# Optimization experiments

Measured on AMD Instinct MI355X. Metric: run time of the kernel, lower is better.

Reference implementation:

```python
import jax, jax.numpy as jnp
import numpy as np

EPS = 1e-6
LN_EPS = 1e-5


def setup_inputs() -> dict:
    key = jax.random.key(0)
    k1, k2, k3 = jax.random.split(key, 3)
    N, L, H, D = 4, 16384, 8, 16
    return {
        "queries": jax.random.normal(k1, (N, L, H, D), dtype=jnp.float32),
        "keys": jax.random.normal(k2, (N, L, H, D), dtype=jnp.float32),
        "values": jax.random.normal(k3, (N, L, H, D), dtype=jnp.float32),
        "ln_gamma": jnp.ones((D,), dtype=jnp.float32),
        "ln_beta": jnp.zeros((D,), dtype=jnp.float32),
    }


def reference(queries, keys, values, ln_gamma, ln_beta):
    initial = values  # [N, L, H, D]
    # to [N, H, L, D] and apply sigmoid feature map
    q = jax.nn.sigmoid(jnp.transpose(queries, (0, 2, 1, 3)))
    k = jax.nn.sigmoid(jnp.transpose(keys, (0, 2, 1, 3)))
    v = jnp.transpose(values, (0, 2, 1, 3))
    L = q.shape[2]
    S = k.shape[2]
    # competition/allocation normalizers (flow attention)
    normalizer_row = 1.0 / jnp.einsum('nhld,nhd->nhl', q + EPS, k.sum(axis=2) + EPS)
    normalizer_col = 1.0 / jnp.einsum('nhsd,nhd->nhs', k + EPS, q.sum(axis=2) + EPS)
    normalizer_row_refine = jnp.einsum(
        'nhld,nhd->nhl', q + EPS, (k * normalizer_col[..., None]).sum(axis=2) + EPS)
    normalizer_col_refine = jnp.einsum(
        'nhsd,nhd->nhs', k + EPS, (q * normalizer_row[..., None]).sum(axis=2) + EPS)
    normalizer_row_refine = jax.nn.sigmoid(normalizer_row_refine * (float(L) / float(S)))
    normalizer_col_refine = jax.nn.softmax(normalizer_col_refine, axis=-1) * S
    # linear attention: K^T @ (V * col_refine), then Q @ kv
    kv = jnp.einsum('nhsd,nhse->nhde', k, v * normalizer_col_refine[..., None])  # [N,H,D,D]
    x = jnp.einsum('nhld,nhde->nhle', q, kv)
    x = x * normalizer_row[..., None] * normalizer_row_refine[..., None]
    x = jnp.transpose(x, (0, 2, 1, 3))  # [N, L, H, D]
    x = initial + x
    # LayerNorm over last dim (D=16), biased variance as in torch
    mean = jnp.mean(x, axis=-1, keepdims=True)
    var = jnp.mean(jnp.square(x - mean), axis=-1, keepdims=True)
    x = (x - mean) / jnp.sqrt(var + LN_EPS) * ln_gamma + ln_beta
    return x
```

## Files before the change

kernel.cpp:

```cpp
#include <hip/hip_runtime.h>
#include <math.h>
#include <stdint.h>

constexpr int LL = 16384;
constexpr int NROW = 65536;
constexpr int NPAIR = NROW * 8;
constexpr int PAIRS_PER_N = NPAIR / 4;
constexpr float EPS = 1e-6f;
constexpr float LN_EPS = 1e-5f;

constexpr int F_KSUM = 0;
constexpr int F_KN   = 512;
constexpr int F_SS   = 1024;
constexpr int F_QSUM = 1056;
constexpr int F_QN   = 1568;
constexpr int F_KV   = 2080;
constexpr int P_A1 = 10272;
constexpr int P_A2 = P_A1 + 2048 * 256;
constexpr int P_KN = P_A2 + 2048 * 128;
constexpr int P_SS = P_KN + 2048 * 128;
constexpr int P_KV = P_SS + 2048 * 8;
constexpr int FLOAT_END = P_KV + 2048 * 2048;
constexpr size_t MIR_Q_BYTE = (size_t)FLOAT_END * 4;
constexpr size_t MIR_ELEMS  = (size_t)NPAIR * 16;
constexpr size_t MIR_K_BYTE = MIR_Q_BYTE + MIR_ELEMS * 2;
constexpr size_t WS_FULL    = MIR_K_BYTE + MIR_ELEMS * 2;

__device__ __forceinline__ float sigm(float x) { return __fdividef(1.f, 1.f + __expf(-x)); }
__device__ __forceinline__ unsigned short f2bf(float f) {
  uint32_t x = __float_as_uint(f);
  return (unsigned short)((x + 0x7FFFu + ((x >> 16) & 1u)) >> 16);
}
__device__ __forceinline__ float bf2f(unsigned short u) {
  return __uint_as_float(((uint32_t)u) << 16);
}

template <bool MIR>
__device__ __forceinline__ void load_sig(const unsigned short* mir, const float* fp, int p, float* r) {
  if (MIR) {
    const uint4* p4 = reinterpret_cast<const uint4*>(mir + (size_t)p * 16);
    uint4 a = p4[0], b = p4[1];
    uint32_t w[8] = {a.x, a.y, a.z, a.w, b.x, b.y, b.z, b.w};
#pragma unroll
    for (int j = 0; j < 8; ++j) {
      r[2 * j]     = bf2f((unsigned short)(w[j] & 0xFFFFu));
      r[2 * j + 1] = bf2f((unsigned short)(w[j] >> 16));
    }
  } else {
    const float4* p4 = reinterpret_cast<const float4*>(fp + (size_t)p * 16);
#pragma unroll
    for (int j = 0; j < 4; ++j) {
      float4 a = p4[j];
      r[4 * j] = sigm(a.x); r[4 * j + 1] = sigm(a.y);
      r[4 * j + 2] = sigm(a.z); r[4 * j + 3] = sigm(a.w);
    }
  }
}
__device__ __forceinline__ void load_raw16(const float* fp, int p, float* r) {
  const float4* p4 = reinterpret_cast<const float4*>(fp + (size_t)p * 16);
#pragma unroll
  for (int j = 0; j < 4; ++j) {
    float4 a = p4[j];
    r[4 * j] = a.x; r[4 * j + 1] = a.y; r[4 * j + 2] = a.z; r[4 * j + 3] = a.w;
  }
}

__device__ __forceinline__ float hred(float v) {
  v += __shfl_xor(v, 8, 64);
  v += __shfl_xor(v, 16, 64);
  v += __shfl_xor(v, 32, 64);
  return v;
}

__device__ __forceinline__ void stat_partial2(float* a, float* b, float* w4 ,
                                              float* dst, int tid) {
  const int wave = tid >> 6, lane = tid & 63;
#pragma unroll
  for (int d = 0; d < 16; ++d) { a[d] = hred(a[d]); b[d] = hred(b[d]); }
  if (lane < 8) {
#pragma unroll
    for (int d = 0; d < 16; ++d) {
      w4[wave * 256 + lane * 16 + d] = a[d];
      w4[wave * 256 + 128 + lane * 16 + d] = b[d];
    }
  }
  __syncthreads();
  dst[tid] = w4[tid] + w4[256 + tid] + w4[512 + tid] + w4[768 + tid];
}

__device__ __forceinline__ void stat_partial1(float* a, float* w1 ,
                                              float* dst, int tid) {
  const int wave = tid >> 6, lane = tid & 63;
#pragma unroll
  for (int d = 0; d < 16; ++d) a[d] = hred(a[d]);
  if (lane < 8) {
#pragma unroll
    for (int d = 0; d < 16; ++d) w1[wave * 128 + lane * 16 + d] = a[d];
  }
  __syncthreads();
  if (tid < 128) dst[tid] = w1[tid] + w1[128 + tid] + w1[256 + tid] + w1[384 + tid];
}

template <bool MIR>
__global__ __launch_bounds__(256) void k_prep(const float* __restrict__ Q, const float* __restrict__ K,
                                              float* __restrict__ ws,
                                              unsigned short* __restrict__ sQ, unsigned short* __restrict__ sK) {
  const int tid = threadIdx.x;
  const int p = blockIdx.x * 256 + tid;
  __shared__ float w4[1024];
  float q[16], k[16];
  load_sig<false>(nullptr, Q, p, q);
  load_sig<false>(nullptr, K, p, k);
  if (MIR) {
    union U { unsigned short u[8]; uint4 v; };
    U a, bb;
#pragma unroll
    for (int j = 0; j < 8; ++j) { a.u[j] = f2bf(q[j]); bb.u[j] = f2bf(q[8 + j]); }
    uint4* dq = reinterpret_cast<uint4*>(sQ + (size_t)p * 16);
    dq[0] = a.v; dq[1] = bb.v;
#pragma unroll
    for (int j = 0; j < 8; ++j) { a.u[j] = f2bf(k[j]); bb.u[j] = f2bf(k[8 + j]); }
    uint4* dk = reinterpret_cast<uint4*>(sK + (size_t)p * 16);
    dk[0] = a.v; dk[1] = bb.v;
  }
  stat_partial2(q, k, w4, ws + P_A1 + (size_t)blockIdx.x * 256, tid);
}

__global__ __launch_bounds__(256) void k_redA(float* __restrict__ ws) {
  const int tid = threadIdx.x;
  const int n = blockIdx.x >> 3, seg = blockIdx.x & 7;
  const int el = tid & 31, sub = tid >> 5;
  __shared__ float w[256];
  const float* src = ws + P_A1 + ((size_t)(n * 512 + sub * 64)) * 256 + seg * 32 + el;
  float a = 0.f;
#pragma unroll
  for (int i = 0; i < 64; ++i) a += src[(size_t)i * 256];
  w[tid] = a;
  __syncthreads();
  if (tid < 128) w[tid] += w[tid + 128];
  __syncthreads();
  if (tid < 64) w[tid] += w[tid + 64];
  __syncthreads();
  if (tid < 32) {
    const float v = w[tid] + w[tid + 32];
    const int elem = seg * 32 + tid;
    if (elem < 128) ws[F_QSUM + n * 128 + elem] = v;
    else ws[F_KSUM + n * 128 + (elem - 128)] = v;
  }
}

template <bool MIR>
__global__ __launch_bounds__(256) void k_refq(const float* __restrict__ Q,
                                              const unsigned short* __restrict__ sQ,
                                              float* __restrict__ ws) {
  const int tid = threadIdx.x;
  const int p = blockIdx.x * 256 + tid;
  const int n = blockIdx.x >> 9;
  __shared__ float ksE[128];
  __shared__ float w1[512];
  if (tid < 128) ksE[tid] = ws[F_KSUM + n * 128 + tid] + EPS;
  __syncthreads();
  const int h = tid & 7;
  float q[16];
  load_sig<MIR>(sQ, Q, p, q);
  float dr = 0.f;
#pragma unroll
  for (int d = 0; d < 16; ++d) dr += (q[d] + EPS) * ksE[h * 16 + d];
  const float nr = __fdividef(1.f, dr);
#pragma unroll
  for (int d = 0; d < 16; ++d) q[d] *= nr;
  stat_partial1(q, w1, ws + P_A2 + (size_t)blockIdx.x * 128, tid);
}

__global__ __launch_bounds__(256) void k_redB(float* __restrict__ ws) {
  const int tid = threadIdx.x;
  const int n = blockIdx.x >> 2, seg = blockIdx.x & 3;
  const int el = tid & 31, sub = tid >> 5;
  __shared__ float w[256];
  const float* src = ws + P_A2 + ((size_t)(n * 512 + sub * 64)) * 128 + seg * 32 + el;
  float a = 0.f;
#pragma unroll
  for (int i = 0; i < 64; ++i) a += src[(size_t)i * 128];
  w[tid] = a;
  __syncthreads();
  if (tid < 128) w[tid] += w[tid + 128];
  __syncthreads();
  if (tid < 64) w[tid] += w[tid + 64];
  __syncthreads();
  if (tid < 32) ws[F_QN + n * 128 + seg * 32 + tid] = w[tid] + w[tid + 32];
}

template <bool MIR>
__global__ __launch_bounds__(256) void k_kv(const float* __restrict__ K, const float* __restrict__ V,
                                            const unsigned short* __restrict__ sK,
                                            float* __restrict__ ws) {
  const int tid = threadIdx.x;
  const int blk = blockIdx.x;
  const int n = blk >> 9;
  constexpr int RS = 132;
  __shared__ float qnE[128], qsE[128];
  __shared__ float ssb[8];
  __shared__ float w1[512];
  __shared__ __align__(16) float kwL[32 * RS];
  __shared__ __align__(16) float vL[32 * RS];
  if (tid < 128) {
    qnE[tid] = ws[F_QN + n * 128 + tid] + EPS;
    qsE[tid] = ws[F_QSUM + n * 128 + tid] + EPS;
  }
  if (tid < 8) ssb[tid] = 0.f;
  __syncthreads();
  const int h = tid & 7, ri = tid >> 3, lane = tid & 63;
  const int h2 = tid >> 5;
  const int d0 = ((tid >> 2) & 7) * 2;
  const int e0 = (tid & 3) * 4;
  const int p = blk * 256 + tid;
  float k[16], v[16];
  load_sig<MIR>(sK, K, p, k);
  load_raw16(V, p, v);
  float dc = 0.f, ncr = 0.f;
#pragma unroll
  for (int d = 0; d < 16; ++d) {
    const float ke = k[d] + EPS;
    dc += ke * qsE[h * 16 + d];
    ncr += ke * qnE[h * 16 + d];
  }
  const float nc = __fdividef(1.f, dc);
  float kn[16];
#pragma unroll
  for (int d = 0; d < 16; ++d) kn[d] = k[d] * nc;
  const float w = __expf(ncr);
  float sw = hred(w);
  if (lane < 8) atomicAdd(&ssb[lane], sw);
  const int wb = ri * RS + h * 16;
#pragma unroll
  for (int d = 0; d < 16; ++d) { kwL[wb + d] = k[d] * w; vL[wb + d] = v[d]; }
  __syncthreads();
  float acc[2][4] = {{0.f, 0.f, 0.f, 0.f}, {0.f, 0.f, 0.f, 0.f}};
  const int rb0 = h2 * 16;
#pragma unroll 4
  for (int r = 0; r < 32; ++r) {
    const int rb = r * RS + rb0;
    const float2 kk = *reinterpret_cast<const float2*>(&kwL[rb + d0]);
    const float4 vv = *reinterpret_cast<const float4*>(&vL[rb + e0]);
    acc[0][0] += kk.x * vv.x; acc[0][1] += kk.x * vv.y;
    acc[0][2] += kk.x * vv.z; acc[0][3] += kk.x * vv.w;
    acc[1][0] += kk.y * vv.x; acc[1][1] += kk.y * vv.y;
    acc[1][2] += kk.y * vv.z; acc[1][3] += kk.y * vv.w;
  }
  __syncthreads();
  stat_partial1(kn, w1, ws + P_KN + (size_t)blk * 128, tid);
  if (tid < 8) ws[P_SS + (size_t)blk * 8 + tid] = ssb[tid];
  float* pk = ws + P_KV + (size_t)blk * 2048;
  *reinterpret_cast<float4*>(pk + h2 * 256 + d0 * 16 + e0) =
      make_float4(acc[0][0], acc[0][1], acc[0][2], acc[0][3]);
  *reinterpret_cast<float4*>(pk + h2 * 256 + (d0 + 1) * 16 + e0) =
      make_float4(acc[1][0], acc[1][1], acc[1][2], acc[1][3]);
}

__global__ __launch_bounds__(256) void k_redC(float* __restrict__ ws) {
  const int tid = threadIdx.x;
  const int blk = blockIdx.x;
  __shared__ float w[256];
  if (blk < 256) {
    const int n = blk >> 6, seg = blk & 63;
    const int el = tid & 31, sub = tid >> 5;
    const float* src = ws + P_KV + ((size_t)(n * 512 + sub * 64)) * 2048 + seg * 32 + el;
    float a = 0.f;
#pragma unroll
    for (int i = 0; i < 64; ++i) a += src[(size_t)i * 2048];
    w[tid] = a;
    __syncthreads();
    if (tid < 128) w[tid] += w[tid + 128];
    __syncthreads();
    if (tid < 64) w[tid] += w[tid + 64];
    __syncthreads();
    if (tid < 32) ws[F_KV + n * 2048 + seg * 32 + tid] = w[tid] + w[tid + 32];
  } else if (blk < 272) {
    const int b2 = blk - 256;
    const int n = b2 >> 2, seg = b2 & 3;
    const int el = tid & 31, sub = tid >> 5;
    const float* src = ws + P_KN + ((size_t)(n * 512 + sub * 64)) * 128 + seg * 32 + el;
    float a = 0.f;
#pragma unroll
    for (int i = 0; i < 64; ++i) a += src[(size_t)i * 128];
    w[tid] = a;
    __syncthreads();
    if (tid < 128) w[tid] += w[tid + 128];
    __syncthreads();
    if (tid < 64) w[tid] += w[tid + 64];
    __syncthreads();
    if (tid < 32) ws[F_KN + n * 128 + seg * 32 + tid] = w[tid] + w[tid + 32];
  } else {
    const int n = blk - 272;
    const int h = tid & 7, sub = tid >> 3;
    const float* src = ws + P_SS + ((size_t)(n * 512 + sub * 16)) * 8 + h;
    float a = 0.f;
#pragma unroll
    for (int i = 0; i < 16; ++i) a += src[(size_t)i * 8];
    w[tid] = a;
    __syncthreads();
    if (tid < 128) w[tid] += w[tid + 128];
    __syncthreads();
    if (tid < 64) w[tid] += w[tid + 64];
    __syncthreads();
    if (tid < 32) w[tid] += w[tid + 32];
    __syncthreads();
    if (tid < 16) w[tid] += w[tid + 16];
    __syncthreads();
    if (tid < 8) ws[F_SS + n * 8 + tid] = w[tid] + w[tid + 8];
  }
}

template <bool MIR>
__global__ __launch_bounds__(256) void k_out(const float* __restrict__ Q, const float* __restrict__ V,
                                             const unsigned short* __restrict__ sQ,
                                             const float* __restrict__ gamma, const float* __restrict__ beta,
                                             const float* __restrict__ ws, float* __restrict__ out) {
  const int tid = threadIdx.x;
  const int p = blockIdx.x * 256 + tid;
  const int n = blockIdx.x >> 9;
  __shared__ __align__(16) float kvs[8 * 260];
  __shared__ float ksE[128], knE[128], gm[16], bt[16], ssE[8];
  if (tid < 8) ssE[tid] = __fdividef((float)LL, ws[F_SS + n * 8 + tid]);
  if (tid >= 8 && tid < 136) {
    const int i = tid - 8;
    ksE[i] = ws[F_KSUM + n * 128 + i] + EPS;
    knE[i] = ws[F_KN + n * 128 + i] + EPS;
  }
  if (tid >= 136 && tid < 152) gm[tid - 136] = gamma[tid - 136];
  else if (tid >= 152 && tid < 168) bt[tid - 152] = beta[tid - 152];
  __syncthreads();
  for (int i = tid; i < 2048; i += 256) {
    const int hh = i >> 8, de = i & 255;
    kvs[hh * 260 + de] = ws[F_KV + n * 2048 + i] * ssE[hh];
  }
  __syncthreads();
  const int h = tid & 7;
  float q[16], v[16];
  load_sig<MIR>(sQ, Q, p, q);
  load_raw16(V, p, v);
  float dr = 0.f, drr = 0.f;
#pragma unroll
  for (int d = 0; d < 16; ++d) {
    const float qe = q[d] + EPS;
    dr += qe * ksE[h * 16 + d];
    drr += qe * knE[h * 16 + d];
  }
  const float sc = __fdividef(1.f, dr) * sigm(drr);
  float x[16];
#pragma unroll
  for (int e = 0; e < 16; ++e) x[e] = 0.f;
#pragma unroll
  for (int d = 0; d < 16; ++d) {
    const float qd = q[d];
    const float4* kr = reinterpret_cast<const float4*>(&kvs[h * 260 + d * 16]);
#pragma unroll
    for (int j = 0; j < 4; ++j) {
      float4 a = kr[j];
      x[4 * j] += qd * a.x; x[4 * j + 1] += qd * a.y;
      x[4 * j + 2] += qd * a.z; x[4 * j + 3] += qd * a.w;
    }
  }
#pragma unroll
  for (int e = 0; e < 16; ++e) x[e] = x[e] * sc + v[e];
  float mean = 0.f;
#pragma unroll
  for (int e = 0; e < 16; ++e) mean += x[e];
  mean *= (1.f / 16.f);
  float var = 0.f;
#pragma unroll
  for (int e = 0; e < 16; ++e) { const float t = x[e] - mean; var += t * t; }
  var *= (1.f / 16.f);
  const float inv = rsqrtf(var + LN_EPS);
#pragma unroll
  for (int e = 0; e < 16; ++e) x[e] = (x[e] - mean) * inv * gm[e] + bt[e];
  float4* op = reinterpret_cast<float4*>(out + (size_t)p * 16);
  op[0] = make_float4(x[0], x[1], x[2], x[3]);
  op[1] = make_float4(x[4], x[5], x[6], x[7]);
  op[2] = make_float4(x[8], x[9], x[10], x[11]);
  op[3] = make_float4(x[12], x[13], x[14], x[15]);
}

extern "C" void kernel_launch(void* const* d_in, const int* in_sizes, int n_in,
                              void* d_out, int out_size, void* d_ws, size_t ws_size,
                              hipStream_t stream) {
  const float* Q = (const float*)d_in[0];
  const float* K = (const float*)d_in[1];
  const float* V = (const float*)d_in[2];
  const float* gamma = (const float*)d_in[3];
  const float* beta = (const float*)d_in[4];
  float* ws = (float*)d_ws;
  float* out = (float*)d_out;
  unsigned short* sQ = (unsigned short*)((char*)d_ws + MIR_Q_BYTE);
  unsigned short* sK = (unsigned short*)((char*)d_ws + MIR_K_BYTE);

  const dim3 blk(256);
  const int gBig = NPAIR / 256;

  if (ws_size >= WS_FULL) {
    k_prep<true><<<gBig, blk, 0, stream>>>(Q, K, ws, sQ, sK);
    k_redA<<<32, blk, 0, stream>>>(ws);
    k_refq<true><<<gBig, blk, 0, stream>>>(Q, sQ, ws);
    k_redB<<<16, blk, 0, stream>>>(ws);
    k_kv<true><<<gBig, blk, 0, stream>>>(K, V, sK, ws);
    k_redC<<<276, blk, 0, stream>>>(ws);
    k_out<true><<<gBig, blk, 0, stream>>>(Q, V, sQ, gamma, beta, ws, out);
  } else {
    k_prep<false><<<gBig, blk, 0, stream>>>(Q, K, ws, nullptr, nullptr);
    k_redA<<<32, blk, 0, stream>>>(ws);
    k_refq<false><<<gBig, blk, 0, stream>>>(Q, nullptr, ws);
    k_redB<<<16, blk, 0, stream>>>(ws);
    k_kv<false><<<gBig, blk, 0, stream>>>(K, V, nullptr, ws);
    k_redC<<<276, blk, 0, stream>>>(ws);
    k_out<false><<<gBig, blk, 0, stream>>>(Q, V, nullptr, gamma, beta, ws, out);
  }
}
```

Measured before the change: 200.6 us.

## Stage per-row global loads and stores through padded LDS for coalescing

Every kernel (prep, refq, kv, out) now loads its 256-row tile of Q/K/V with consecutive threads reading consecutive float4/uint2 chunks into a padded LDS buffer, then each thread reads its own 16-element row from LDS. The bf16 mirror writes and the final output stores take the same route in reverse. Before, each thread read and wrote a 64-byte row stride. The aim is fully coalesced global access, paid for with extra LDS traffic, more __syncthreads, and larger shared-memory use that may lower occupancy.

After: 206.7 us. 1.03x slower.

```diff
diff --git a/kernel.cpp b/kernel.cpp
--- a/kernel.cpp
+++ b/kernel.cpp
@@ -5,9 +5,9 @@
 constexpr int LL = 16384;
 constexpr int NROW = 65536;
 constexpr int NPAIR = NROW * 8;
-constexpr int PAIRS_PER_N = NPAIR / 4;
 constexpr float EPS = 1e-6f;
 constexpr float LN_EPS = 1e-5f;
+constexpr size_t MIR_ELEMS = (size_t)NPAIR * 16;
 
 constexpr int F_KSUM = 0;
 constexpr int F_KN   = 512;
@@ -22,9 +22,9 @@
 constexpr int P_KV = P_SS + 2048 * 8;
 constexpr int FLOAT_END = P_KV + 2048 * 2048;
 constexpr size_t MIR_Q_BYTE = (size_t)FLOAT_END * 4;
-constexpr size_t MIR_ELEMS  = (size_t)NPAIR * 16;
 constexpr size_t MIR_K_BYTE = MIR_Q_BYTE + MIR_ELEMS * 2;
 constexpr size_t WS_FULL    = MIR_K_BYTE + MIR_ELEMS * 2;
+
 
 __device__ __forceinline__ float sigm(float x) { return __fdividef(1.f, 1.f + __expf(-x)); }
 __device__ __forceinline__ unsigned short f2bf(float f) {
@@ -35,33 +35,42 @@
   return __uint_as_float(((uint32_t)u) << 16);
 }
 
-template <bool MIR>
-__device__ __forceinline__ void load_sig(const unsigned short* mir, const float* fp, int p, float* r) {
-  if (MIR) {
-    const uint4* p4 = reinterpret_cast<const uint4*>(mir + (size_t)p * 16);
-    uint4 a = p4[0], b = p4[1];
-    uint32_t w[8] = {a.x, a.y, a.z, a.w, b.x, b.y, b.z, b.w};
-#pragma unroll
-    for (int j = 0; j < 8; ++j) {
-      r[2 * j]     = bf2f((unsigned short)(w[j] & 0xFFFFu));
-      r[2 * j + 1] = bf2f((unsigned short)(w[j] >> 16));
-    }
-  } else {
-    const float4* p4 = reinterpret_cast<const float4*>(fp + (size_t)p * 16);
-#pragma unroll
-    for (int j = 0; j < 4; ++j) {
-      float4 a = p4[j];
-      r[4 * j] = sigm(a.x); r[4 * j + 1] = sigm(a.y);
-      r[4 * j + 2] = sigm(a.z); r[4 * j + 3] = sigm(a.w);
-    }
-  }
-}
-__device__ __forceinline__ void load_raw16(const float* fp, int p, float* r) {
-  const float4* p4 = reinterpret_cast<const float4*>(fp + (size_t)p * 16);
-#pragma unroll
-  for (int j = 0; j < 4; ++j) {
-    float4 a = p4[j];
-    r[4 * j] = a.x; r[4 * j + 1] = a.y; r[4 * j + 2] = a.z; r[4 * j + 3] = a.w;
+
+__device__ __forceinline__ void stage_f32(const float* src, int pairBase, float* lds, int tid) {
+  const float4* s4 = reinterpret_cast<const float4*>(src) + (size_t)pairBase * 4;
+#pragma unroll
+  for (int i = 0; i < 4; ++i) {
+    const int G = i * 256 + tid;
+    const float4 v = s4[G];
+    float* r = lds + (G >> 2) * 17 + (G & 3) * 4;
+    r[0] = v.x; r[1] = v.y; r[2] = v.z; r[3] = v.w;
+  }
+}
+
+__device__ __forceinline__ void stage_bf16(const unsigned short* mir, int pairBase, float* lds, int tid) {
+  const uint2* s2 = reinterpret_cast<const uint2*>(mir) + (size_t)pairBase * 4;
+#pragma unroll
+  for (int i = 0; i < 4; ++i) {
+    const int G = i * 256 + tid;
+    const uint2 u = s2[G];
+    float* r = lds + (G >> 2) * 17 + (G & 3) * 4;
+    r[0] = bf2f((unsigned short)(u.x & 0xFFFFu)); r[1] = bf2f((unsigned short)(u.x >> 16));
+    r[2] = bf2f((unsigned short)(u.y & 0xFFFFu)); r[3] = bf2f((unsigned short)(u.y >> 16));
+  }
+}
+
+__device__ __forceinline__ void mirror_store(unsigned short* mir, int pairBase, uint32_t* ldsu,
+                                             const float* q, int tid) {
+#pragma unroll
+  for (int j = 0; j < 8; ++j)
+    ldsu[tid * 9 + j] = (uint32_t)f2bf(q[2 * j]) | ((uint32_t)f2bf(q[2 * j + 1]) << 16);
+  __syncthreads();
+  uint2* d2 = reinterpret_cast<uint2*>(mir) + (size_t)pairBase * 4;
+#pragma unroll
+  for (int i = 0; i < 4; ++i) {
+    const int G = i * 256 + tid;
+    const int pl = G >> 2, qd = G & 3;
+    d2[G] = make_uint2(ldsu[pl * 9 + qd * 2], ldsu[pl * 9 + qd * 2 + 1]);
   }
 }
 
@@ -106,24 +115,29 @@
                                               float* __restrict__ ws,
                                               unsigned short* __restrict__ sQ, unsigned short* __restrict__ sK) {
   const int tid = threadIdx.x;
-  const int p = blockIdx.x * 256 + tid;
-  __shared__ float w4[1024];
+  const int pairBase = blockIdx.x * 256;
+  __shared__ __align__(16) float A[4352];
+  uint32_t* Au = reinterpret_cast<uint32_t*>(A);
   float q[16], k[16];
-  load_sig<false>(nullptr, Q, p, q);
-  load_sig<false>(nullptr, K, p, k);
+  stage_f32(Q, pairBase, A, tid);
+  __syncthreads();
+#pragma unroll
+  for (int d = 0; d < 16; ++d) q[d] = sigm(A[tid * 17 + d]);
+  __syncthreads();
   if (MIR) {
-    union U { unsigned short u[8]; uint4 v; };
-    U a, bb;
-#pragma unroll
-    for (int j = 0; j < 8; ++j) { a.u[j] = f2bf(q[j]); bb.u[j] = f2bf(q[8 + j]); }
-    uint4* dq = reinterpret_cast<uint4*>(sQ + (size_t)p * 16);
-    dq[0] = a.v; dq[1] = bb.v;
-#pragma unroll
-    for (int j = 0; j < 8; ++j) { a.u[j] = f2bf(k[j]); bb.u[j] = f2bf(k[8 + j]); }
-    uint4* dk = reinterpret_cast<uint4*>(sK + (size_t)p * 16);
-    dk[0] = a.v; dk[1] = bb.v;
-  }
-  stat_partial2(q, k, w4, ws + P_A1 + (size_t)blockIdx.x * 256, tid);
+    mirror_store(sQ, pairBase, Au, q, tid);
+    __syncthreads();
+  }
+  stage_f32(K, pairBase, A, tid);
+  __syncthreads();
+#pragma unroll
+  for (int d = 0; d < 16; ++d) k[d] = sigm(A[tid * 17 + d]);
+  __syncthreads();
+  if (MIR) {
+    mirror_store(sK, pairBase, Au, k, tid);
+    __syncthreads();
+  }
+  stat_partial2(q, k, A, ws + P_A1 + (size_t)blockIdx.x * 256, tid);
 }
 
 __global__ __launch_bounds__(256) void k_redA(float* __restrict__ ws) {
@@ -154,22 +168,29 @@
                                               const unsigned short* __restrict__ sQ,
                                               float* __restrict__ ws) {
   const int tid = threadIdx.x;
-  const int p = blockIdx.x * 256 + tid;
+  const int pairBase = blockIdx.x * 256;
   const int n = blockIdx.x >> 9;
+  __shared__ __align__(16) float A[4352];
   __shared__ float ksE[128];
   __shared__ float w1[512];
+  if (MIR) stage_bf16(sQ, pairBase, A, tid);
+  else     stage_f32(Q, pairBase, A, tid);
   if (tid < 128) ksE[tid] = ws[F_KSUM + n * 128 + tid] + EPS;
   __syncthreads();
   const int h = tid & 7;
-  float q[16];
-  load_sig<MIR>(sQ, Q, p, q);
+  float qv[16];
+#pragma unroll
+  for (int d = 0; d < 16; ++d) {
+    const float t = A[tid * 17 + d];
+    qv[d] = MIR ? t : sigm(t);
+  }
   float dr = 0.f;
 #pragma unroll
-  for (int d = 0; d < 16; ++d) dr += (q[d] + EPS) * ksE[h * 16 + d];
+  for (int d = 0; d < 16; ++d) dr += (qv[d] + EPS) * ksE[h * 16 + d];
   const float nr = __fdividef(1.f, dr);
 #pragma unroll
-  for (int d = 0; d < 16; ++d) q[d] *= nr;
-  stat_partial1(q, w1, ws + P_A2 + (size_t)blockIdx.x * 128, tid);
+  for (int d = 0; d < 16; ++d) qv[d] *= nr;
+  stat_partial1(qv, w1, ws + P_A2 + (size_t)blockIdx.x * 128, tid);
 }
 
 __global__ __launch_bounds__(256) void k_redB(float* __restrict__ ws) {
@@ -200,23 +221,59 @@
   constexpr int RS = 132;
   __shared__ float qnE[128], qsE[128];
   __shared__ float ssb[8];
-  __shared__ float w1[512];
   __shared__ __align__(16) float kwL[32 * RS];
   __shared__ __align__(16) float vL[32 * RS];
+  const int pairBase = blk * 256;
+  if (MIR) {
+    const uint2* s2 = reinterpret_cast<const uint2*>(sK) + (size_t)pairBase * 4;
+#pragma unroll
+    for (int i = 0; i < 4; ++i) {
+      const int G = i * 256 + tid;
+      const uint2 u = s2[G];
+      const int p = G >> 2;
+      float* r = &kwL[(p >> 3) * RS + (p & 7) * 16 + (G & 3) * 4];
+      r[0] = bf2f((unsigned short)(u.x & 0xFFFFu)); r[1] = bf2f((unsigned short)(u.x >> 16));
+      r[2] = bf2f((unsigned short)(u.y & 0xFFFFu)); r[3] = bf2f((unsigned short)(u.y >> 16));
+    }
+  } else {
+    const float4* s4 = reinterpret_cast<const float4*>(K) + (size_t)pairBase * 4;
+#pragma unroll
+    for (int i = 0; i < 4; ++i) {
+      const int G = i * 256 + tid;
+      const float4 v4 = s4[G];
+      const int p = G >> 2;
+      float* r = &kwL[(p >> 3) * RS + (p & 7) * 16 + (G & 3) * 4];
+      r[0] = v4.x; r[1] = v4.y; r[2] = v4.z; r[3] = v4.w;
+    }
+  }
+  {
+    const float4* s4 = reinterpret_cast<const float4*>(V) + (size_t)pairBase * 4;
+#pragma unroll
+    for (int i = 0; i < 4; ++i) {
+      const int G = i * 256 + tid;
+      const float4 v4 = s4[G];
+      const int p = G >> 2;
+      float* r = &vL[(p >> 3) * RS + (p & 7) * 16 + (G & 3) * 4];
+      r[0] = v4.x; r[1] = v4.y; r[2] = v4.z; r[3] = v4.w;
+    }
+  }
   if (tid < 128) {
     qnE[tid] = ws[F_QN + n * 128 + tid] + EPS;
     qsE[tid] = ws[F_QSUM + n * 128 + tid] + EPS;
   }
   if (tid < 8) ssb[tid] = 0.f;
   __syncthreads();
-  const int h = tid & 7, ri = tid >> 3, lane = tid & 63;
+  const int h = tid & 7, lane = tid & 63;
   const int h2 = tid >> 5;
   const int d0 = ((tid >> 2) & 7) * 2;
   const int e0 = (tid & 3) * 4;
-  const int p = blk * 256 + tid;
-  float k[16], v[16];
-  load_sig<MIR>(sK, K, p, k);
-  load_raw16(V, p, v);
+  const int myrow = (tid >> 3) * RS + h * 16;
+  float k[16];
+#pragma unroll
+  for (int d = 0; d < 16; ++d) {
+    const float t = kwL[myrow + d];
+    k[d] = MIR ? t : sigm(t);
+  }
   float dc = 0.f, ncr = 0.f;
 #pragma unroll
   for (int d = 0; d < 16; ++d) {
@@ -231,9 +288,8 @@
   const float w = __expf(ncr);
   float sw = hred(w);
   if (lane < 8) atomicAdd(&ssb[lane], sw);
-  const int wb = ri * RS + h * 16;
-#pragma unroll
-  for (int d = 0; d < 16; ++d) { kwL[wb + d] = k[d] * w; vL[wb + d] = v[d]; }
+#pragma unroll
+  for (int d = 0; d < 16; ++d) kwL[myrow + d] = k[d] * w;
   __syncthreads();
   float acc[2][4] = {{0.f, 0.f, 0.f, 0.f}, {0.f, 0.f, 0.f, 0.f}};
   const int rb0 = h2 * 16;
@@ -248,7 +304,7 @@
     acc[1][2] += kk.y * vv.z; acc[1][3] += kk.y * vv.w;
   }
   __syncthreads();
-  stat_partial1(kn, w1, ws + P_KN + (size_t)blk * 128, tid);
+  stat_partial1(kn, kwL, ws + P_KN + (size_t)blk * 128, tid);
   if (tid < 8) ws[P_SS + (size_t)blk * 8 + tid] = ssb[tid];
   float* pk = ws + P_KV + (size_t)blk * 2048;
   *reinterpret_cast<float4*>(pk + h2 * 256 + d0 * 16 + e0) =
@@ -292,8 +348,8 @@
     if (tid < 32) ws[F_KN + n * 128 + seg * 32 + tid] = w[tid] + w[tid + 32];
   } else {
     const int n = blk - 272;
-    const int h = tid & 7, sub = tid >> 3;
-    const float* src = ws + P_SS + ((size_t)(n * 512 + sub * 16)) * 8 + h;
+    const int hh = tid & 7, sub = tid >> 3;
+    const float* src = ws + P_SS + ((size_t)(n * 512 + sub * 16)) * 8 + hh;
     float a = 0.f;
 #pragma unroll
     for (int i = 0; i < 16; ++i) a += src[(size_t)i * 8];
@@ -317,10 +373,13 @@
                                              const float* __restrict__ gamma, const float* __restrict__ beta,
                                              const float* __restrict__ ws, float* __restrict__ out) {
   const int tid = threadIdx.x;
-  const int p = blockIdx.x * 256 + tid;
+  const int pairBase = blockIdx.x * 256;
   const int n = blockIdx.x >> 9;
+  __shared__ __align__(16) float S[4352];
   __shared__ __align__(16) float kvs[8 * 260];
   __shared__ float ksE[128], knE[128], gm[16], bt[16], ssE[8];
+  if (MIR) stage_bf16(sQ, pairBase, S, tid);
+  else     stage_f32(Q, pairBase, S, tid);
   if (tid < 8) ssE[tid] = __fdividef((float)LL, ws[F_SS + n * 8 + tid]);
   if (tid >= 8 && tid < 136) {
     const int i = tid - 8;
@@ -334,11 +393,19 @@
     const int hh = i >> 8, de = i & 255;
     kvs[hh * 260 + de] = ws[F_KV + n * 2048 + i] * ssE[hh];
   }
-  __syncthreads();
   const int h = tid & 7;
-  float q[16], v[16];
-  load_sig<MIR>(sQ, Q, p, q);
-  load_raw16(V, p, v);
+  float q[16];
+#pragma unroll
+  for (int d = 0; d < 16; ++d) {
+    const float t = S[tid * 17 + d];
+    q[d] = MIR ? t : sigm(t);
+  }
+  __syncthreads();
+  stage_f32(V, pairBase, S, tid);
+  __syncthreads();
+  float v[16];
+#pragma unroll
+  for (int d = 0; d < 16; ++d) v[d] = S[tid * 17 + d];
   float dr = 0.f, drr = 0.f;
 #pragma unroll
   for (int d = 0; d < 16; ++d) {
@@ -374,11 +441,16 @@
   const float inv = rsqrtf(var + LN_EPS);
 #pragma unroll
   for (int e = 0; e < 16; ++e) x[e] = (x[e] - mean) * inv * gm[e] + bt[e];
-  float4* op = reinterpret_cast<float4*>(out + (size_t)p * 16);
-  op[0] = make_float4(x[0], x[1], x[2], x[3]);
-  op[1] = make_float4(x[4], x[5], x[6], x[7]);
-  op[2] = make_float4(x[8], x[9], x[10], x[11]);
-  op[3] = make_float4(x[12], x[13], x[14], x[15]);
+#pragma unroll
+  for (int d = 0; d < 16; ++d) S[tid * 17 + d] = x[d];
+  __syncthreads();
+  float4* o4 = reinterpret_cast<float4*>(out) + (size_t)pairBase * 4;
+#pragma unroll
+  for (int i = 0; i < 4; ++i) {
+    const int G = i * 256 + tid;
+    const float* r = &S[(G >> 2) * 17 + (G & 3) * 4];
+    o4[G] = make_float4(r[0], r[1], r[2], r[3]);
+  }
 }
 
 extern "C" void kernel_launch(void* const* d_in, const int* in_sizes, int n_in,
```
